# Kernel optimization log

Measured on AMD Instinct MI355X. Metric: run time of the kernel, lower is better.

The kernel has to match this reference:

```python
import jax, jax.numpy as jnp
import numpy as np

N = 8192   # nodes per modality
D = 128    # hidden_channels
H = 2      # transformer heads
R = 15     # relations in HeteroConv (use_speaker='no')
E = 16384  # edges per relation
L = 2      # num_layers
# relation src/dst node-type ids: 0=audio, 1=text, 2=visual (dict order: a/v/t past, a/v/t future, a/v/t self, then cross)
SRC = np.array([0, 2, 1, 0, 2, 1, 0, 2, 1, 0, 0, 2, 2, 1, 1])
DST = np.array([0, 2, 1, 0, 2, 1, 0, 2, 1, 2, 1, 0, 1, 0, 2])


def setup_inputs() -> dict:
    key = jax.random.key(0)
    ks = jax.random.split(key, 18)
    f = lambda k, sh: jax.random.normal(k, sh, dtype=jnp.float32) * 0.05
    return {
        "x_audio": jax.random.normal(ks[0], (N, D), jnp.float32),
        "x_text": jax.random.normal(ks[1], (N, D), jnp.float32),
        "x_visual": jax.random.normal(ks[2], (N, D), jnp.float32),
        "edge_index": jax.random.randint(ks[3], (R, 2, E), 0, N, jnp.int32),
        "Wrel": f(ks[4], (L, R, D, D)),
        "brel": f(ks[5], (L, R, D)),
        "Wroot": f(ks[6], (L, R, D, D)),
        "Wq": f(ks[7], (D, H * D)), "bq": f(ks[8], (H * D,)),
        "Wk": f(ks[9], (D, H * D)), "bk": f(ks[10], (H * D,)),
        "Wv": f(ks[11], (D, H * D)), "bv": f(ks[12], (H * D,)),
        "Wskip": f(ks[13], (D, D)), "bskip": f(ks[14], (D,)),
        "gamma": jnp.ones((D,), jnp.float32),
        "beta": jnp.zeros((D,), jnp.float32),
    }


def reference(x_audio, x_text, x_visual, edge_index, Wrel, brel, Wroot,
              Wq, bq, Wk, bk, Wv, bv, Wskip, bskip, gamma, beta):
    src_t = jnp.asarray(SRC)
    dst_t = jnp.asarray(DST)
    x = jnp.stack([x_audio, x_text, x_visual])           # [3, N, D]
    src_idx = edge_index[:, 0]                            # [R, E]
    dst_idx = edge_index[:, 1]                            # [R, E]
    rel = jnp.arange(R)

    # --- HeteroConv of 15 GraphConvs (aggr='add' inside, 'mean' over the 5 relations per dst type) ---
    seg = (rel[:, None] * N + dst_idx).reshape(-1)        # per-relation segment ids
    for l in range(L):
        feats = jnp.take_along_axis(x[src_t], src_idx[:, :, None], axis=1)     # [R, E, D]
        msg = jax.ops.segment_sum(feats.reshape(R * E, D), seg,
                                  num_segments=R * N).reshape(R, N, D)          # scatter-add per relation
        out = (jnp.einsum('rnd,rde->rne', msg, Wrel[l]) + brel[l][:, None, :]
               + jnp.einsum('rnd,rde->rne', x[dst_t], Wroot[l]))                # lin_rel(agg) + lin_root(x_dst)
        x = jax.nn.relu(jnp.zeros_like(x).at[dst_t].add(out) / 5.0)            # mean over 5 relations per dst

    # --- hetero_to_homo: concat audio, text, visual (offsets 0, N, 2N) ---
    hx = x.reshape(3 * N, D)
    src_h = (src_t[:, None] * N + src_idx).reshape(-1)    # [R*E]
    dst_h = (dst_t[:, None] * N + dst_idx).reshape(-1)

    # --- TransformerConv (concat=False -> head mean, root skip) ---
    q = (hx @ Wq + bq).reshape(3 * N, H, D)
    k = (hx @ Wk + bk).reshape(3 * N, H, D)
    v = (hx @ Wv + bv).reshape(3 * N, H, D)
    logits = jnp.einsum('ehd,ehd->eh', q[dst_h], k[src_h]) / jnp.sqrt(jnp.float32(D))
    m = jax.ops.segment_max(logits, dst_h, num_segments=3 * N)
    p = jnp.exp(logits - m[dst_h])
    denom = jax.ops.segment_sum(p, dst_h, num_segments=3 * N)
    alpha = p / denom[dst_h]                              # segment softmax over incoming edges
    agg = jax.ops.segment_sum(alpha[:, :, None] * v[src_h], dst_h, num_segments=3 * N)  # [3N, H, D]
    out = agg.mean(axis=1) + hx @ Wskip + bskip

    # --- BatchNorm1d (training-mode batch stats) + leaky_relu ---
    mu = out.mean(axis=0)
    var = ((out - mu) ** 2).mean(axis=0)
    y = (out - mu) / jnp.sqrt(var + 1e-5) * gamma + beta
    y = jax.nn.leaky_relu(y)                              # negative_slope=0.01 (torch default)
    return y.reshape(3, N, D)                             # [audio, text, visual]
```

## Files before the change

kernel.cpp:

```cpp
#include <hip/hip_runtime.h>
#include <hip/hip_bf16.h>

#define NN 8192
#define DD 128
#define HH 2
#define RR 15
#define EE 16384
#define NLAYER 2
#define NMOD 3
#define TN (NMOD*NN)
#define NE (RR*EE)
#define SCB (TN/256)

#define SRC_BITS 0x16818618u
#define DST_BITS 0x21198618u
__device__ __forceinline__ int srcOf(int r) { return (SRC_BITS >> (2 * r)) & 3; }
__device__ __forceinline__ int dstOf(int r) { return (DST_BITS >> (2 * r)) & 3; }

typedef __attribute__((ext_vector_type(8))) short bf16x8;
typedef __attribute__((ext_vector_type(4))) float f32x4;
typedef _Float16 h2 __attribute__((ext_vector_type(2)));

__device__ __forceinline__ unsigned short f2bf(float v) {
    union { float f; unsigned int u; } x; x.f = v;
    unsigned int r = (x.u + 0x7fffu + ((x.u >> 16) & 1u)) >> 16;
    return (unsigned short)r;
}
__device__ __forceinline__ float bf2f(unsigned int bits16) {
    return __uint_as_float(bits16 << 16);
}
__device__ __forceinline__ void bfu4(uint4 u, float* f) {
    f[0] = bf2f(u.x & 0xffffu); f[1] = bf2f(u.x >> 16);
    f[2] = bf2f(u.y & 0xffffu); f[3] = bf2f(u.y >> 16);
    f[4] = bf2f(u.z & 0xffffu); f[5] = bf2f(u.z >> 16);
    f[6] = bf2f(u.w & 0xffffu); f[7] = bf2f(u.w >> 16);
}

__device__ __forceinline__ float dot8_f16(uint4 a, uint4 b, float acc) {
#if __has_builtin(__builtin_amdgcn_fdot2)
    acc = __builtin_amdgcn_fdot2(__builtin_bit_cast(h2, a.x), __builtin_bit_cast(h2, b.x), acc, false);
    acc = __builtin_amdgcn_fdot2(__builtin_bit_cast(h2, a.y), __builtin_bit_cast(h2, b.y), acc, false);
    acc = __builtin_amdgcn_fdot2(__builtin_bit_cast(h2, a.z), __builtin_bit_cast(h2, b.z), acc, false);
    acc = __builtin_amdgcn_fdot2(__builtin_bit_cast(h2, a.w), __builtin_bit_cast(h2, b.w), acc, false);
#else
    h2 av, bv;
    av = __builtin_bit_cast(h2, a.x); bv = __builtin_bit_cast(h2, b.x);
    acc += (float)av.x * (float)bv.x + (float)av.y * (float)bv.y;
    av = __builtin_bit_cast(h2, a.y); bv = __builtin_bit_cast(h2, b.y);
    acc += (float)av.x * (float)bv.x + (float)av.y * (float)bv.y;
    av = __builtin_bit_cast(h2, a.z); bv = __builtin_bit_cast(h2, b.z);
    acc += (float)av.x * (float)bv.x + (float)av.y * (float)bv.y;
    av = __builtin_bit_cast(h2, a.w); bv = __builtin_bit_cast(h2, b.w);
    acc += (float)av.x * (float)bv.x + (float)av.y * (float)bv.y;
#endif
    return acc;
}

__global__ __launch_bounds__(256) void prep_all(
        const float* __restrict__ Wrel, const float* __restrict__ Wroot,
        const float* __restrict__ brel,
        const float* __restrict__ Wq, const float* __restrict__ Wk,
        const float* __restrict__ Wv, const float* __restrict__ Wskip,
        const float* __restrict__ xa, const float* __restrict__ xt,
        const float* __restrict__ xv,
        unsigned short* __restrict__ WrelT, unsigned short* __restrict__ WsumT,
        float* __restrict__ bsum,
        unsigned short* __restrict__ WqT, unsigned short* __restrict__ WkT,
        unsigned short* __restrict__ WvT, unsigned short* __restrict__ WskipT,
        unsigned short* __restrict__ xb, int* __restrict__ cnt) {
    int y = blockIdx.y;
    int t = blockIdx.x * 256 + threadIdx.x;
    if (y < 30) {
        int k = t >> 7, c = t & 127;
        WrelT[(size_t)y * 16384 + c * 128 + k] = f2bf(Wrel[(size_t)y * 16384 + t]);
    } else if (y < 36) {
        int mat = y - 30, l = mat / 3, m = mat % 3;
        int k = t >> 7, c = t & 127;
        float s = 0.f;
        #pragma unroll
        for (int r = 0; r < RR; r++)
            if (((DST_BITS >> (2 * r)) & 3) == (unsigned)m) s += Wroot[(size_t)(l * RR + r) * 16384 + t];
        WsumT[(size_t)mat * 16384 + c * 128 + k] = f2bf(s);
        if (blockIdx.x == 0 && threadIdx.x < 128) {
            float b = 0.f;
            #pragma unroll
            for (int r = 0; r < RR; r++)
                if (((DST_BITS >> (2 * r)) & 3) == (unsigned)m) b += brel[(l * RR + r) * 128 + threadIdx.x];
            bsum[mat * 128 + threadIdx.x] = b;
        }
    } else if (y < 39) {
        int which = y - 36;
        const float* s = which == 0 ? Wq : which == 1 ? Wk : Wv;
        unsigned short* d = which == 0 ? WqT : which == 1 ? WkT : WvT;
        #pragma unroll
        for (int it = 0; it < 2; it++) {
            int tt = t + it * 16384;
            int k = tt >> 8, c = tt & 255;
            d[c * 128 + k] = f2bf(s[tt]);
        }
    } else if (y == 39) {
        int k = t >> 7, c = t & 127;
        WskipT[c * 128 + k] = f2bf(Wskip[t]);
    } else if (y == 40) {
        for (int i = t; i < TN + 256; i += 16384) cnt[i] = 0;
    } else {
        int m = y - 41;
        const float* s = m == 0 ? xa : m == 1 ? xt : xv;
        unsigned short* d = xb + (size_t)m * NN * DD;
        for (int i = t * 4; i < NN * DD; i += 16384 * 4) {
            float4 v = *(const float4*)(s + i);
            uint2 o;
            o.x = (unsigned)f2bf(v.x) | ((unsigned)f2bf(v.y) << 16);
            o.y = (unsigned)f2bf(v.z) | ((unsigned)f2bf(v.w) << 16);
            *(uint2*)(d + i) = o;
        }
    }
}

__global__ void count_edges(const int* __restrict__ edge, int* __restrict__ cnt) {
    int t = blockIdx.x * 256 + threadIdx.x;
    if (t >= NE) return;
    int r = t >> 14, e = t & (EE - 1);
    int dst = edge[r * 2 * EE + EE + e];
    atomicAdd(&cnt[dstOf(r) * NN + dst], 1);
}

__global__ __launch_bounds__(256) void scan_reduce(const int* __restrict__ cnt,
                                                   int* __restrict__ part) {
    int t = threadIdx.x;
    int v = cnt[blockIdx.x * 256 + t];
    #pragma unroll
    for (int off = 32; off >= 1; off >>= 1) v += __shfl_xor(v, off);
    __shared__ int ws[4];
    if ((t & 63) == 0) ws[t >> 6] = v;
    __syncthreads();
    if (t == 0) part[blockIdx.x] = ws[0] + ws[1] + ws[2] + ws[3];
}

__global__ __launch_bounds__(128) void scan_mid(int* __restrict__ part, int* __restrict__ startA) {
    __shared__ int lds[128];
    int t = threadIdx.x;
    int v = (t < SCB) ? part[t] : 0;
    lds[t] = v;
    __syncthreads();
    for (int off = 1; off < 128; off <<= 1) {
        int u = (t >= off) ? lds[t - off] : 0;
        __syncthreads();
        lds[t] += u;
        __syncthreads();
    }
    if (t < SCB) part[t] = lds[t] - v;
    if (t == 0) startA[TN] = NE;
}

__global__ __launch_bounds__(256) void scan_final(const int* __restrict__ cnt,
                                                  const int* __restrict__ part,
                                                  int* __restrict__ startA,
                                                  int* __restrict__ cursor) {
    int t = threadIdx.x;
    int lane = t & 63, w = t >> 6;
    int i = blockIdx.x * 256 + t;
    int v = cnt[i];
    int inc = v;
    #pragma unroll
    for (int off = 1; off < 64; off <<= 1) {
        int u = __shfl_up(inc, off);
        if (lane >= off) inc += u;
    }
    __shared__ int wtot[4];
    if (lane == 63) wtot[w] = inc;
    __syncthreads();
    int wofs = 0;
    #pragma unroll
    for (int j = 0; j < 4; j++) if (j < w) wofs += wtot[j];
    int ex = part[blockIdx.x] + wofs + inc - v;
    startA[i] = ex;
    cursor[i] = ex;
}

__global__ void place_edges(const int* __restrict__ edge, int* __restrict__ cursor,
                            unsigned int* __restrict__ sorted) {
    int t = blockIdx.x * 256 + threadIdx.x;
    if (t >= NE) return;
    int r = t >> 14, e = t & (EE - 1);
    int src = edge[r * 2 * EE + e];
    int dst = edge[r * 2 * EE + EE + e];
    int pos = atomicAdd(&cursor[dstOf(r) * NN + dst], 1);
    unsigned int zrow = ((unsigned int)r << 13) | (unsigned int)src;
    unsigned int srch = (unsigned int)(srcOf(r) * NN + src);
    sorted[pos] = (zrow << 15) | srch;
}

template<int MODE>
__device__ __forceinline__ void gemm_tile(const unsigned short* __restrict__ A,
                                          const unsigned short* __restrict__ BT,
                                          const float* __restrict__ bias,
                                          void* __restrict__ Cout,
                                          int ldc, int colofs, int row0,
                                          unsigned short* lds, float oscale = 1.f) {
    unsigned short* Alds = lds;
    unsigned short* Blds = lds + 16384;
    const int tid = threadIdx.x;
    const int lane = tid & 63;
    const int w = tid >> 6;
    #pragma unroll
    for (int i = 0; i < 8; i++) {
        int c = i * 256 + tid;
        int row = c >> 4;
        int k0 = (c & 15) << 3;
        uint4 va = *(const uint4*)(A + (size_t)(row0 + row) * 128 + k0);
        *(uint4*)((char*)Alds + (((row * 256 + k0 * 2)) ^ ((row & 7) << 4))) = va;
        uint4 vb = *(const uint4*)(BT + (size_t)row * 128 + k0);
        *(uint4*)((char*)Blds + (((row * 256 + k0 * 2)) ^ ((row & 7) << 4))) = vb;
    }
    __syncthreads();
    f32x4 acc[2][8];
    #pragma unroll
    for (int mi = 0; mi < 2; mi++)
        #pragma unroll
        for (int nj = 0; nj < 8; nj++) acc[mi][nj] = (f32x4){0.f, 0.f, 0.f, 0.f};
    const int lr = lane & 15, lk = lane >> 4;
    #pragma unroll
    for (int ks = 0; ks < 4; ks++) {
        bf16x8 a[2], b[8];
        #pragma unroll
        for (int mi = 0; mi < 2; mi++) {
            int row = w * 32 + mi * 16 + lr;
            a[mi] = *(const bf16x8*)((char*)Alds + ((row * 256 + (ks * 32 + lk * 8) * 2) ^ ((row & 7) << 4)));
        }
        #pragma unroll
        for (int nj = 0; nj < 8; nj++) {
            int row = nj * 16 + lr;
            b[nj] = *(const bf16x8*)((char*)Blds + ((row * 256 + (ks * 32 + lk * 8) * 2) ^ ((row & 7) << 4)));
        }
        #pragma unroll
        for (int mi = 0; mi < 2; mi++)
            #pragma unroll
            for (int nj = 0; nj < 8; nj++)
                acc[mi][nj] = __builtin_amdgcn_mfma_f32_16x16x32_bf16(a[mi], b[nj], acc[mi][nj], 0, 0, 0);
    }
    __syncthreads();
    float* Clds = (float*)lds;
    #pragma unroll
    for (int mi = 0; mi < 2; mi++) {
        #pragma unroll
        for (int nj = 0; nj < 8; nj++) {
            int ccl = nj * 16 + lr;
            float bb = bias ? bias[ccl] : 0.f;
            #pragma unroll
            for (int r = 0; r < 4; r++) {
                int row = w * 32 + mi * 16 + lk * 4 + r;
                Clds[row * 128 + ccl] = acc[mi][nj][r] + bb;
            }
        }
    }
    __syncthreads();
    #pragma unroll
    for (int p = 0; p < 8; p++) {
        int row = p * 16 + (tid >> 4);
        int c0 = (tid & 15) * 8;
        float4 fa = *(const float4*)(Clds + row * 128 + c0);
        float4 fb = *(const float4*)(Clds + row * 128 + c0 + 4);
        if (MODE == 2) {
            unsigned r0 = (unsigned)f2bf(fa.x) | ((unsigned)f2bf(fa.y) << 16);
            unsigned r1 = (unsigned)f2bf(fa.z) | ((unsigned)f2bf(fa.w) << 16);
            unsigned r2 = (unsigned)f2bf(fb.x) | ((unsigned)f2bf(fb.y) << 16);
            unsigned r3 = (unsigned)f2bf(fb.z) | ((unsigned)f2bf(fb.w) << 16);
            uint4 pk = {r0, r1, r2, r3};
            *(uint4*)((unsigned short*)Cout + (size_t)(row0 + row) * ldc + colofs + c0) = pk;
        } else if (MODE == 3) {
            unsigned r0 = __builtin_bit_cast(unsigned, __builtin_amdgcn_cvt_pkrtz(fa.x * oscale, fa.y * oscale));
            unsigned r1 = __builtin_bit_cast(unsigned, __builtin_amdgcn_cvt_pkrtz(fa.z * oscale, fa.w * oscale));
            unsigned r2 = __builtin_bit_cast(unsigned, __builtin_amdgcn_cvt_pkrtz(fb.x * oscale, fb.y * oscale));
            unsigned r3 = __builtin_bit_cast(unsigned, __builtin_amdgcn_cvt_pkrtz(fb.z * oscale, fb.w * oscale));
            uint4 pk = {r0, r1, r2, r3};
            *(uint4*)((unsigned short*)Cout + (size_t)(row0 + row) * ldc + colofs + c0) = pk;
        } else {
            float* Cf = (float*)Cout;
            *(float4*)(Cf + (size_t)(row0 + row) * ldc + colofs + c0) = fa;
            *(float4*)(Cf + (size_t)(row0 + row) * ldc + colofs + c0 + 4) = fb;
        }
    }
}

__global__ __launch_bounds__(256) void zroot_gemm(const unsigned short* __restrict__ xbf,
                                                  const unsigned short* __restrict__ WrelT_l,
                                                  const unsigned short* __restrict__ WrootSumT_l,
                                                  const float* __restrict__ brelSum_l,
                                                  unsigned short* __restrict__ z,
                                                  unsigned short* __restrict__ xroot) {
    __shared__ unsigned short lds[2 * 16384];
    int y = blockIdx.y;
    if (y < RR) {
        gemm_tile<2>(xbf + (size_t)srcOf(y) * NN * 128, WrelT_l + (size_t)y * 16384, nullptr,
                     z + (size_t)y * NN * 128, 128, 0, blockIdx.x * 128, lds);
    } else {
        int m = y - RR;
        gemm_tile<2>(xbf + (size_t)m * NN * 128, WrootSumT_l + (size_t)m * 16384, brelSum_l + m * 128,
                     xroot + (size_t)m * NN * 128, 128, 0, blockIdx.x * 128, lds);
    }
}

__global__ __launch_bounds__(256) void qkvskip_gemm(const unsigned short* __restrict__ xbf,
                                                    const unsigned short* __restrict__ WqT,
                                                    const unsigned short* __restrict__ WkT,
                                                    const unsigned short* __restrict__ WvT,
                                                    const unsigned short* __restrict__ WskipT,
                                                    const float* __restrict__ bq,
                                                    const float* __restrict__ bk,
                                                    const float* __restrict__ bv,
                                                    const float* __restrict__ bskip,
                                                    unsigned short* __restrict__ qb,
                                                    unsigned short* __restrict__ kb,
                                                    unsigned short* __restrict__ vb,
                                                    float* __restrict__ out) {
    __shared__ unsigned short lds[2 * 16384];
    int y = blockIdx.y;
    if (y < 4) {
        int which = y >> 1, half = y & 1;
        const unsigned short* BT = (which == 0 ? WqT : WkT) + half * 16384;
        const float* bias = (which == 0 ? bq : bk) + half * 128;
        unsigned short* C = (which == 0 ? qb : kb);
        float os = (which == 0) ? 0.08838834764831845f : 1.f;
        gemm_tile<3>(xbf, BT, bias, C, 256, half * 128, blockIdx.x * 128, lds, os);
    } else if (y < 6) {
        int half = y & 1;
        gemm_tile<2>(xbf, WvT + half * 16384, bv + half * 128, vb, 256, half * 128, blockIdx.x * 128, lds);
    } else {
        gemm_tile<0>(xbf, WskipT, bskip, out, 128, 0, blockIdx.x * 128, lds);
    }
}

__global__ __launch_bounds__(256) void gather_relu(const unsigned short* __restrict__ z,
                                                   const unsigned short* __restrict__ xroot,
                                                   const unsigned int* __restrict__ sorted,
                                                   const int* __restrict__ startA,
                                                   unsigned short* __restrict__ xout) {
    int node = blockIdx.x * 4 + (threadIdx.x >> 6);
    int lane = threadIdx.x & 63;
    int g = lane >> 4, p = lane & 15;
    int st = startA[node], en = startA[node + 1];
    float acc[8];
    #pragma unroll
    for (int j = 0; j < 8; j++) acc[j] = 0.f;
    int idx = st + g;
    unsigned int vcur = (idx < en) ? sorted[idx] : 0u;
    for (int base = st; base < en; base += 4) {
        unsigned int vnext = (idx + 4 < en) ? sorted[idx + 4] : 0u;
        uint4 u = *(const uint4*)(z + ((size_t)(vcur >> 15) << 7) + p * 8);
        if (idx < en) {
            float f[8]; bfu4(u, f);
            #pragma unroll
            for (int j = 0; j < 8; j++) acc[j] += f[j];
        }
        vcur = vnext;
        idx += 4;
    }
    #pragma unroll
    for (int j = 0; j < 8; j++) {
        acc[j] += __shfl_xor(acc[j], 32);
        acc[j] += __shfl_xor(acc[j], 16);
    }
    if (g == 0) {
        uint4 rt = *(const uint4*)(xroot + ((size_t)node << 7) + p * 8);
        float r[8]; bfu4(rt, r);
        unsigned short o[8];
        #pragma unroll
        for (int j = 0; j < 8; j++) {
            float v = (r[j] + acc[j]) * 0.2f;
            o[j] = f2bf(v > 0.f ? v : 0.f);
        }
        uint4 pk;
        pk.x = (unsigned)o[0] | ((unsigned)o[1] << 16);
        pk.y = (unsigned)o[2] | ((unsigned)o[3] << 16);
        pk.z = (unsigned)o[4] | ((unsigned)o[5] << 16);
        pk.w = (unsigned)o[6] | ((unsigned)o[7] << 16);
        *(uint4*)(xout + ((size_t)node << 7) + p * 8) = pk;
    }
}

__global__ __launch_bounds__(256) void attn_fused(const unsigned short* __restrict__ qb,
                                                  const unsigned short* __restrict__ kb,
                                                  const unsigned short* __restrict__ vb,
                                                  const unsigned int* __restrict__ sorted,
                                                  const int* __restrict__ startA,
                                                  float* __restrict__ out) {
    int node = blockIdx.x * 4 + (threadIdx.x >> 6);
    int lane = threadIdx.x & 63;
    int g = lane >> 4, p = lane & 15;
    uint4 q0 = *(const uint4*)(qb + (size_t)node * 256 + p * 8);
    uint4 q1 = *(const uint4*)(qb + (size_t)node * 256 + 128 + p * 8);
    float s0 = 0.f, s1 = 0.f;
    float a0[8], a1[8];
    #pragma unroll
    for (int j = 0; j < 8; j++) { a0[j] = 0.f; a1[j] = 0.f; }
    int st = startA[node], en = startA[node + 1];
    int idx = st + g;
    unsigned int vcur = (idx < en) ? sorted[idx] : 0u;
    for (int base = st; base < en; base += 4) {
        unsigned int vnext = (idx + 4 < en) ? sorted[idx + 4] : 0u;
        bool valid = idx < en;
        int srch = (int)(vcur & 32767u);
        const unsigned short* krow = kb + (size_t)srch * 256;
        const unsigned short* vrow = vb + (size_t)srch * 256;
        uint4 k0r = *(const uint4*)(krow + p * 8);
        uint4 k1r = *(const uint4*)(krow + 128 + p * 8);
        uint4 v0r = *(const uint4*)(vrow + p * 8);
        uint4 v1r = *(const uint4*)(vrow + 128 + p * 8);
        float d0 = dot8_f16(q0, k0r, 0.f);
        float d1 = dot8_f16(q1, k1r, 0.f);
        #pragma unroll
        for (int off = 8; off >= 1; off >>= 1) {
            d0 += __shfl_xor(d0, off);
            d1 += __shfl_xor(d1, off);
        }
        float p0 = valid ? __expf(d0) : 0.f;
        float p1 = valid ? __expf(d1) : 0.f;
        s0 += p0; s1 += p1;
        float v0[8], v1[8];
        bfu4(v0r, v0); bfu4(v1r, v1);
        #pragma unroll
        for (int j = 0; j < 8; j++) {
            a0[j] += p0 * v0[j];
            a1[j] += p1 * v1[j];
        }
        vcur = vnext;
        idx += 4;
    }
    #pragma unroll
    for (int off = 32; off >= 16; off >>= 1) {
        s0 += __shfl_xor(s0, off);
        s1 += __shfl_xor(s1, off);
        #pragma unroll
        for (int j = 0; j < 8; j++) {
            a0[j] += __shfl_xor(a0[j], off);
            a1[j] += __shfl_xor(a1[j], off);
        }
    }
    if (g == 0) {
        float inv0 = (s0 > 0.f) ? 0.5f / s0 : 0.f;
        float inv1 = (s1 > 0.f) ? 0.5f / s1 : 0.f;
        float* op = out + (size_t)node * 128 + p * 8;
        float4 ska = *(const float4*)op;
        float4 skb = *(const float4*)(op + 4);
        float4 ra, rb;
        ra.x = a0[0] * inv0 + a1[0] * inv1 + ska.x;
        ra.y = a0[1] * inv0 + a1[1] * inv1 + ska.y;
        ra.z = a0[2] * inv0 + a1[2] * inv1 + ska.z;
        ra.w = a0[3] * inv0 + a1[3] * inv1 + ska.w;
        rb.x = a0[4] * inv0 + a1[4] * inv1 + skb.x;
        rb.y = a0[5] * inv0 + a1[5] * inv1 + skb.y;
        rb.z = a0[6] * inv0 + a1[6] * inv1 + skb.z;
        rb.w = a0[7] * inv0 + a1[7] * inv1 + skb.w;
        *(float4*)op = ra;
        *(float4*)(op + 4) = rb;
    }
}

__global__ void colstats(const float* __restrict__ outb, float* __restrict__ stats) {
    int col = threadIdx.x & 127;
    int sub = threadIdx.x >> 7;
    float s = 0.f, ss = 0.f;
    for (int row = blockIdx.x * 2 + sub; row < TN; row += gridDim.x * 2) {
        float vv = outb[(size_t)row * DD + col];
        s += vv;
        ss += vv * vv;
    }
    __shared__ float red[2][256];
    red[0][threadIdx.x] = s;
    red[1][threadIdx.x] = ss;
    __syncthreads();
    if (sub == 0) {
        s  += red[0][threadIdx.x + 128];
        ss += red[1][threadIdx.x + 128];
        atomicAdd(&stats[col], s);
        atomicAdd(&stats[DD + col], ss);
    }
}

__global__ void ln_act(float* __restrict__ outb, const float* __restrict__ stats,
                       const float* __restrict__ gamma, const float* __restrict__ beta) {
    int i = (blockIdx.x * 256 + threadIdx.x) * 4;
    if (i >= TN * DD) return;
    int col = i & 127;
    float4 v = *(const float4*)(outb + i);
    float o[4] = {v.x, v.y, v.z, v.w};
    #pragma unroll
    for (int j = 0; j < 4; j++) {
        int c = col + j;
        float mu = stats[c] * (1.f / TN);
        float var = stats[DD + c] * (1.f / TN) - mu * mu;
        float inv = rsqrtf(var + 1e-5f);
        float vv = (o[j] - mu) * inv * gamma[c] + beta[c];
        o[j] = vv > 0.f ? vv : 0.01f * vv;
    }
    float4 res = {o[0], o[1], o[2], o[3]};
    *(float4*)(outb + i) = res;
}

extern "C" void kernel_launch(void* const* d_in, const int* in_sizes, int n_in,
                              void* d_out, int out_size, void* d_ws, size_t ws_size,
                              hipStream_t stream) {
    const float* x_audio = (const float*)d_in[0];
    const float* x_text  = (const float*)d_in[1];
    const float* x_vis   = (const float*)d_in[2];
    const int*   edge    = (const int*)d_in[3];
    const float* Wrel    = (const float*)d_in[4];
    const float* brel    = (const float*)d_in[5];
    const float* Wroot   = (const float*)d_in[6];
    const float* Wq      = (const float*)d_in[7];
    const float* bq      = (const float*)d_in[8];
    const float* Wk      = (const float*)d_in[9];
    const float* bk      = (const float*)d_in[10];
    const float* Wv      = (const float*)d_in[11];
    const float* bv      = (const float*)d_in[12];
    const float* Wskip   = (const float*)d_in[13];
    const float* bskip   = (const float*)d_in[14];
    const float* gamma   = (const float*)d_in[15];
    const float* beta    = (const float*)d_in[16];
    float* out = (float*)d_out;

    char* p = (char*)d_ws;
    unsigned short* xbfA = (unsigned short*)p; p += (size_t)TN * 128 * 2;
    unsigned short* xbfB = (unsigned short*)p; p += (size_t)TN * 128 * 2;
    unsigned short* zqkv = (unsigned short*)p; p += (size_t)3 * TN * 256 * 2;
    unsigned short* z  = zqkv;
    unsigned short* qb = zqkv;
    unsigned short* kb = zqkv + (size_t)TN * 256;
    unsigned short* vb = zqkv + (size_t)2 * TN * 256;
    unsigned short* xroot = (unsigned short*)p; p += (size_t)TN * 128 * 2;
    unsigned short* WrelT = (unsigned short*)p; p += (size_t)2 * RR * 16384 * 2;
    unsigned short* WrootSumT = (unsigned short*)p; p += (size_t)6 * 16384 * 2;
    float* brelSum = (float*)p; p += 6 * 128 * 4;
    unsigned short* WqT = (unsigned short*)p; p += 256 * 128 * 2;
    unsigned short* WkT = (unsigned short*)p; p += 256 * 128 * 2;
    unsigned short* WvT = (unsigned short*)p; p += 256 * 128 * 2;
    unsigned short* WskipT = (unsigned short*)p; p += 128 * 128 * 2;
    unsigned int* sorted = (unsigned int*)p; p += (size_t)NE * 4;
    int* startA = (int*)p; p += (TN + 4) * 4;
    int* cursor = (int*)p; p += (TN + 4) * 4;
    int* cnt = (int*)p; p += TN * 4;
    float* stats = (float*)p; p += 256 * 4;
    int* part = (int*)p; p += SCB * 4;
    size_t needed = (size_t)(p - (char*)d_ws);
    if (ws_size < needed) return;

    prep_all<<<dim3(64, 44), 256, 0, stream>>>(Wrel, Wroot, brel, Wq, Wk, Wv, Wskip,
                                               x_audio, x_text, x_vis,
                                               WrelT, WrootSumT, brelSum,
                                               WqT, WkT, WvT, WskipT, xbfA, cnt);

    count_edges<<<NE / 256, 256, 0, stream>>>(edge, cnt);
    scan_reduce<<<SCB, 256, 0, stream>>>(cnt, part);
    scan_mid<<<1, 128, 0, stream>>>(part, startA);
    scan_final<<<SCB, 256, 0, stream>>>(cnt, part, startA, cursor);
    place_edges<<<NE / 256, 256, 0, stream>>>(edge, cursor, sorted);

    unsigned short* xcur = xbfA;
    unsigned short* xnxt = xbfB;
    for (int l = 0; l < NLAYER; ++l) {
        zroot_gemm<<<dim3(NN / 128, RR + NMOD), 256, 0, stream>>>(
            xcur, WrelT + (size_t)l * RR * 16384, WrootSumT + (size_t)l * NMOD * 16384,
            brelSum + l * NMOD * 128, z, xroot);
        gather_relu<<<TN / 4, 256, 0, stream>>>(z, xroot, sorted, startA, xnxt);
        unsigned short* t = xcur; xcur = xnxt; xnxt = t;
    }

    qkvskip_gemm<<<dim3(TN / 128, 7), 256, 0, stream>>>(xcur, WqT, WkT, WvT, WskipT,
                                                        bq, bk, bv, bskip, qb, kb, vb, out);
    attn_fused<<<TN / 4, 256, 0, stream>>>(qb, kb, vb, sorted, startA, out);

    colstats<<<384, 256, 0, stream>>>(out, stats);
    ln_act<<<(TN * DD) / 1024, 256, 0, stream>>>(out, stats, gamma, beta);
}
```

Before: 202.2 us.

## Switch bf16 storage to fp16, fold edge counting and scan-mid into neighbors

```diff
diff --git a/kernel.cpp b/kernel.cpp
--- a/kernel.cpp
+++ b/kernel.cpp
@@ -17,23 +17,15 @@
 __device__ __forceinline__ int srcOf(int r) { return (SRC_BITS >> (2 * r)) & 3; }
 __device__ __forceinline__ int dstOf(int r) { return (DST_BITS >> (2 * r)) & 3; }
 
-typedef __attribute__((ext_vector_type(8))) short bf16x8;
+typedef __attribute__((ext_vector_type(8))) _Float16 f16x8;
 typedef __attribute__((ext_vector_type(4))) float f32x4;
 typedef _Float16 h2 __attribute__((ext_vector_type(2)));
 
-__device__ __forceinline__ unsigned short f2bf(float v) {
-    union { float f; unsigned int u; } x; x.f = v;
-    unsigned int r = (x.u + 0x7fffu + ((x.u >> 16) & 1u)) >> 16;
-    return (unsigned short)r;
-}
-__device__ __forceinline__ float bf2f(unsigned int bits16) {
-    return __uint_as_float(bits16 << 16);
-}
-__device__ __forceinline__ void bfu4(uint4 u, float* f) {
-    f[0] = bf2f(u.x & 0xffffu); f[1] = bf2f(u.x >> 16);
-    f[2] = bf2f(u.y & 0xffffu); f[3] = bf2f(u.y >> 16);
-    f[4] = bf2f(u.z & 0xffffu); f[5] = bf2f(u.z >> 16);
-    f[6] = bf2f(u.w & 0xffffu); f[7] = bf2f(u.w >> 16);
+__device__ __forceinline__ unsigned short f2h(float v) {
+    return __builtin_bit_cast(unsigned short, (_Float16)v);
+}
+__device__ __forceinline__ unsigned int pkh(float a, float b) {
+    return __builtin_bit_cast(unsigned int, __builtin_amdgcn_cvt_pkrtz(a, b));
 }
 
 __device__ __forceinline__ float dot8_f16(uint4 a, uint4 b, float acc) {
@@ -56,13 +48,17 @@
     return acc;
 }
 
+__device__ __forceinline__ h2 h2shfl_xor(h2 a, int off) {
+    return __builtin_bit_cast(h2, __shfl_xor(__builtin_bit_cast(int, a), off));
+}
+
 __global__ __launch_bounds__(256) void prep_all(
         const float* __restrict__ Wrel, const float* __restrict__ Wroot,
         const float* __restrict__ brel,
         const float* __restrict__ Wq, const float* __restrict__ Wk,
         const float* __restrict__ Wv, const float* __restrict__ Wskip,
         const float* __restrict__ xa, const float* __restrict__ xt,
-        const float* __restrict__ xv,
+        const float* __restrict__ xv, const int* __restrict__ edge,
         unsigned short* __restrict__ WrelT, unsigned short* __restrict__ WsumT,
         float* __restrict__ bsum,
         unsigned short* __restrict__ WqT, unsigned short* __restrict__ WkT,
@@ -72,7 +68,7 @@
     int t = blockIdx.x * 256 + threadIdx.x;
     if (y < 30) {
         int k = t >> 7, c = t & 127;
-        WrelT[(size_t)y * 16384 + c * 128 + k] = f2bf(Wrel[(size_t)y * 16384 + t]);
+        WrelT[(size_t)y * 16384 + c * 128 + k] = f2h(Wrel[(size_t)y * 16384 + t]);
     } else if (y < 36) {
         int mat = y - 30, l = mat / 3, m = mat % 3;
         int k = t >> 7, c = t & 127;
@@ -80,7 +76,7 @@
         #pragma unroll
         for (int r = 0; r < RR; r++)
             if (((DST_BITS >> (2 * r)) & 3) == (unsigned)m) s += Wroot[(size_t)(l * RR + r) * 16384 + t];
-        WsumT[(size_t)mat * 16384 + c * 128 + k] = f2bf(s);
+        WsumT[(size_t)mat * 16384 + c * 128 + k] = f2h(s);
         if (blockIdx.x == 0 && threadIdx.x < 128) {
             float b = 0.f;
             #pragma unroll
@@ -96,33 +92,28 @@
         for (int it = 0; it < 2; it++) {
             int tt = t + it * 16384;
             int k = tt >> 8, c = tt & 255;
-            d[c * 128 + k] = f2bf(s[tt]);
+            d[c * 128 + k] = f2h(s[tt]);
         }
     } else if (y == 39) {
         int k = t >> 7, c = t & 127;
-        WskipT[c * 128 + k] = f2bf(Wskip[t]);
-    } else if (y == 40) {
-        for (int i = t; i < TN + 256; i += 16384) cnt[i] = 0;
-    } else {
-        int m = y - 41;
+        WskipT[c * 128 + k] = f2h(Wskip[t]);
+    } else if (y < 43) {
+        int m = y - 40;
         const float* s = m == 0 ? xa : m == 1 ? xt : xv;
         unsigned short* d = xb + (size_t)m * NN * DD;
         for (int i = t * 4; i < NN * DD; i += 16384 * 4) {
             float4 v = *(const float4*)(s + i);
             uint2 o;
-            o.x = (unsigned)f2bf(v.x) | ((unsigned)f2bf(v.y) << 16);
-            o.y = (unsigned)f2bf(v.z) | ((unsigned)f2bf(v.w) << 16);
+            o.x = pkh(v.x, v.y);
+            o.y = pkh(v.z, v.w);
             *(uint2*)(d + i) = o;
         }
-    }
-}
-
-__global__ void count_edges(const int* __restrict__ edge, int* __restrict__ cnt) {
-    int t = blockIdx.x * 256 + threadIdx.x;
-    if (t >= NE) return;
-    int r = t >> 14, e = t & (EE - 1);
-    int dst = edge[r * 2 * EE + EE + e];
-    atomicAdd(&cnt[dstOf(r) * NN + dst], 1);
+    } else {
+        int id = (y - 43) * 16384 + t;
+        int r = id >> 14, e = id & (EE - 1);
+        int dst = edge[r * 2 * EE + EE + e];
+        atomicAdd(&cnt[dstOf(r) * NN + dst], 1);
+    }
 }
 
 __global__ __launch_bounds__(256) void scan_reduce(const int* __restrict__ cnt,
@@ -137,28 +128,20 @@
     if (t == 0) part[blockIdx.x] = ws[0] + ws[1] + ws[2] + ws[3];
 }
 
-__global__ __launch_bounds__(128) void scan_mid(int* __restrict__ part, int* __restrict__ startA) {
-    __shared__ int lds[128];
-    int t = threadIdx.x;
-    int v = (t < SCB) ? part[t] : 0;
-    lds[t] = v;
-    __syncthreads();
-    for (int off = 1; off < 128; off <<= 1) {
-        int u = (t >= off) ? lds[t - off] : 0;
-        __syncthreads();
-        lds[t] += u;
-        __syncthreads();
-    }
-    if (t < SCB) part[t] = lds[t] - v;
-    if (t == 0) startA[TN] = NE;
-}
-
 __global__ __launch_bounds__(256) void scan_final(const int* __restrict__ cnt,
                                                   const int* __restrict__ part,
                                                   int* __restrict__ startA,
                                                   int* __restrict__ cursor) {
+    __shared__ int pofs;
     int t = threadIdx.x;
     int lane = t & 63, w = t >> 6;
+    if (t < 64) {
+        int s = 0;
+        for (int j = t; j < SCB; j += 64) s += (j < (int)blockIdx.x) ? part[j] : 0;
+        #pragma unroll
+        for (int off = 32; off >= 1; off >>= 1) s += __shfl_xor(s, off);
+        if (t == 0) pofs = s;
+    }
     int i = blockIdx.x * 256 + t;
     int v = cnt[i];
     int inc = v;
@@ -173,9 +156,10 @@
     int wofs = 0;
     #pragma unroll
     for (int j = 0; j < 4; j++) if (j < w) wofs += wtot[j];
-    int ex = part[blockIdx.x] + wofs + inc - v;
+    int ex = pofs + wofs + inc - v;
     startA[i] = ex;
     cursor[i] = ex;
+    if (i == TN - 1) startA[TN] = NE;
 }
 
 __global__ void place_edges(const int* __restrict__ edge, int* __restrict__ cursor,
@@ -222,22 +206,22 @@
     const int lr = lane & 15, lk = lane >> 4;
     #pragma unroll
     for (int ks = 0; ks < 4; ks++) {
-        bf16x8 a[2], b[8];
+        f16x8 a[2], b[8];
         #pragma unroll
         for (int mi = 0; mi < 2; mi++) {
             int row = w * 32 + mi * 16 + lr;
-            a[mi] = *(const bf16x8*)((char*)Alds + ((row * 256 + (ks * 32 + lk * 8) * 2) ^ ((row & 7) << 4)));
+            a[mi] = *(const f16x8*)((char*)Alds + ((row * 256 + (ks * 32 + lk * 8) * 2) ^ ((row & 7) << 4)));
         }
         #pragma unroll
         for (int nj = 0; nj < 8; nj++) {
             int row = nj * 16 + lr;
-            b[nj] = *(const bf16x8*)((char*)Blds + ((row * 256 + (ks * 32 + lk * 8) * 2) ^ ((row & 7) << 4)));
+            b[nj] = *(const f16x8*)((char*)Blds + ((row * 256 + (ks * 32 + lk * 8) * 2) ^ ((row & 7) << 4)));
         }
         #pragma unroll
         for (int mi = 0; mi < 2; mi++)
             #pragma unroll
             for (int nj = 0; nj < 8; nj++)
-                acc[mi][nj] = __builtin_amdgcn_mfma_f32_16x16x32_bf16(a[mi], b[nj], acc[mi][nj], 0, 0, 0);
+                acc[mi][nj] = __builtin_amdgcn_mfma_f32_16x16x32_f16(a[mi], b[nj], acc[mi][nj], 0, 0, 0);
     }
     __syncthreads();
     float* Clds = (float*)lds;
@@ -261,19 +245,12 @@
         int c0 = (tid & 15) * 8;
         float4 fa = *(const float4*)(Clds + row * 128 + c0);
         float4 fb = *(const float4*)(Clds + row * 128 + c0 + 4);
-        if (MODE == 2) {
-            unsigned r0 = (unsigned)f2bf(fa.x) | ((unsigned)f2bf(fa.y) << 16);
-            unsigned r1 = (unsigned)f2bf(fa.z) | ((unsigned)f2bf(fa.w) << 16);
-            unsigned r2 = (unsigned)f2bf(fb.x) | ((unsigned)f2bf(fb.y) << 16);
-            unsigned r3 = (unsigned)f2bf(fb.z) | ((unsigned)f2bf(fb.w) << 16);
-            uint4 pk = {r0, r1, r2, r3};
-            *(uint4*)((unsigned short*)Cout + (size_t)(row0 + row) * ldc + colofs + c0) = pk;
-        } else if (MODE == 3) {
-            unsigned r0 = __builtin_bit_cast(unsigned, __builtin_amdgcn_cvt_pkrtz(fa.x * oscale, fa.y * oscale));
-            unsigned r1 = __builtin_bit_cast(unsigned, __builtin_amdgcn_cvt_pkrtz(fa.z * oscale, fa.w * oscale));
-            unsigned r2 = __builtin_bit_cast(unsigned, __builtin_amdgcn_cvt_pkrtz(fb.x * oscale, fb.y * oscale));
-            unsigned r3 = __builtin_bit_cast(unsigned, __builtin_amdgcn_cvt_pkrtz(fb.z * oscale, fb.w * oscale));
-            uint4 pk = {r0, r1, r2, r3};
+        if (MODE == 3) {
+            uint4 pk;
+            pk.x = pkh(fa.x * oscale, fa.y * oscale);
+            pk.y = pkh(fa.z * oscale, fa.w * oscale);
+            pk.z = pkh(fb.x * oscale, fb.y * oscale);
+            pk.w = pkh(fb.z * oscale, fb.w * oscale);
             *(uint4*)((unsigned short*)Cout + (size_t)(row0 + row) * ldc + colofs + c0) = pk;
         } else {
             float* Cf = (float*)Cout;
@@ -292,11 +269,11 @@
     __shared__ unsigned short lds[2 * 16384];
     int y = blockIdx.y;
     if (y < RR) {
-        gemm_tile<2>(xbf + (size_t)srcOf(y) * NN * 128, WrelT_l + (size_t)y * 16384, nullptr,
+        gemm_tile<3>(xbf + (size_t)srcOf(y) * NN * 128, WrelT_l + (size_t)y * 16384, nullptr,
                      z + (size_t)y * NN * 128, 128, 0, blockIdx.x * 128, lds);
     } else {
         int m = y - RR;
-        gemm_tile<2>(xbf + (size_t)m * NN * 128, WrootSumT_l + (size_t)m * 16384, brelSum_l + m * 128,
+        gemm_tile<3>(xbf + (size_t)m * NN * 128, WrootSumT_l + (size_t)m * 16384, brelSum_l + m * 128,
                      xroot + (size_t)m * NN * 128, 128, 0, blockIdx.x * 128, lds);
     }
 }
@@ -316,16 +293,13 @@
                                                     float* __restrict__ out) {
     __shared__ unsigned short lds[2 * 16384];
     int y = blockIdx.y;
-    if (y < 4) {
+    if (y < 6) {
         int which = y >> 1, half = y & 1;
-        const unsigned short* BT = (which == 0 ? WqT : WkT) + half * 16384;
-        const float* bias = (which == 0 ? bq : bk) + half * 128;
-        unsigned short* C = (which == 0 ? qb : kb);
+        const unsigned short* BT = (which == 0 ? WqT : which == 1 ? WkT : WvT) + half * 16384;
+        const float* bias = (which == 0 ? bq : which == 1 ? bk : bv) + half * 128;
+        unsigned short* C = (which == 0 ? qb : which == 1 ? kb : vb);
         float os = (which == 0) ? 0.08838834764831845f : 1.f;
         gemm_tile<3>(xbf, BT, bias, C, 256, half * 128, blockIdx.x * 128, lds, os);
-    } else if (y < 6) {
-        int half = y & 1;
-        gemm_tile<2>(xbf, WvT + half * 16384, bv + half * 128, vb, 256, half * 128, blockIdx.x * 128, lds);
     } else {
         gemm_tile<0>(xbf, WskipT, bskip, out, 128, 0, blockIdx.x * 128, lds);
     }
@@ -340,41 +314,43 @@
     int lane = threadIdx.x & 63;
     int g = lane >> 4, p = lane & 15;
     int st = startA[node], en = startA[node + 1];
-    float acc[8];
-    #pragma unroll
-    for (int j = 0; j < 8; j++) acc[j] = 0.f;
+    h2 acc[4];
+    #pragma unroll
+    for (int j = 0; j < 4; j++) acc[j] = (h2){0, 0};
     int idx = st + g;
     unsigned int vcur = (idx < en) ? sorted[idx] : 0u;
     for (int base = st; base < en; base += 4) {
         unsigned int vnext = (idx + 4 < en) ? sorted[idx + 4] : 0u;
         uint4 u = *(const uint4*)(z + ((size_t)(vcur >> 15) << 7) + p * 8);
         if (idx < en) {
-            float f[8]; bfu4(u, f);
-            #pragma unroll
-            for (int j = 0; j < 8; j++) acc[j] += f[j];
+            acc[0] += __builtin_bit_cast(h2, u.x);
+            acc[1] += __builtin_bit_cast(h2, u.y);
+            acc[2] += __builtin_bit_cast(h2, u.z);
+            acc[3] += __builtin_bit_cast(h2, u.w);
         }
         vcur = vnext;
         idx += 4;
     }
     #pragma unroll
-    for (int j = 0; j < 8; j++) {
-        acc[j] += __shfl_xor(acc[j], 32);
-        acc[j] += __shfl_xor(acc[j], 16);
+    for (int j = 0; j < 4; j++) {
+        acc[j] += h2shfl_xor(acc[j], 32);
+        acc[j] += h2shfl_xor(acc[j], 16);
     }
     if (g == 0) {
         uint4 rt = *(const uint4*)(xroot + ((size_t)node << 7) + p * 8);
-        float r[8]; bfu4(rt, r);
-        unsigned short o[8];
-        #pragma unroll
-        for (int j = 0; j < 8; j++) {
-            float v = (r[j] + acc[j]) * 0.2f;
-            o[j] = f2bf(v > 0.f ? v : 0.f);
-        }
+        h2 r[4];
+        r[0] = __builtin_bit_cast(h2, rt.x);
+        r[1] = __builtin_bit_cast(h2, rt.y);
+        r[2] = __builtin_bit_cast(h2, rt.z);
+        r[3] = __builtin_bit_cast(h2, rt.w);
         uint4 pk;
-        pk.x = (unsigned)o[0] | ((unsigned)o[1] << 16);
-        pk.y = (unsigned)o[2] | ((unsigned)o[3] << 16);
-        pk.z = (unsigned)o[4] | ((unsigned)o[5] << 16);
-        pk.w = (unsigned)o[6] | ((unsigned)o[7] << 16);
+        unsigned int* po = (unsigned int*)&pk;
+        #pragma unroll
+        for (int j = 0; j < 4; j++) {
+            float v0 = ((float)r[j].x + (float)acc[j].x) * 0.2f;
+            float v1 = ((float)r[j].y + (float)acc[j].y) * 0.2f;
+            po[j] = pkh(v0 > 0.f ? v0 : 0.f, v1 > 0.f ? v1 : 0.f);
+        }
         *(uint4*)(xout + ((size_t)node << 7) + p * 8) = pk;
     }
 }
@@ -391,9 +367,9 @@
     uint4 q0 = *(const uint4*)(qb + (size_t)node * 256 + p * 8);
     uint4 q1 = *(const uint4*)(qb + (size_t)node * 256 + 128 + p * 8);
     float s0 = 0.f, s1 = 0.f;
-    float a0[8], a1[8];
-    #pragma unroll
-    for (int j = 0; j < 8; j++) { a0[j] = 0.f; a1[j] = 0.f; }
+    h2 a0h[4], a1h[4];
+    #pragma unroll
+    for (int jj = 0; jj < 4; jj++) { a0h[jj] = (h2){0, 0}; a1h[jj] = (h2){0, 0}; }
     int st = startA[node], en = startA[node + 1];
     int idx = st + g;
     unsigned int vcur = (idx < en) ? sorted[idx] : 0u;
@@ -417,13 +393,16 @@
         float p0 = valid ? __expf(d0) : 0.f;
         float p1 = valid ? __expf(d1) : 0.f;
         s0 += p0; s1 += p1;
-        float v0[8], v1[8];
-        bfu4(v0r, v0); bfu4(v1r, v1);
-        #pragma unroll
-        for (int j = 0; j < 8; j++) {
-            a0[j] += p0 * v0[j];
-            a1[j] += p1 * v1[j];
-        }
+        h2 ph0 = (h2){(_Float16)p0, (_Float16)p0};
+        h2 ph1 = (h2){(_Float16)p1, (_Float16)p1};
+        a0h[0] += ph0 * __builtin_bit_cast(h2, v0r.x);
+        a0h[1] += ph0 * __builtin_bit_cast(h2, v0r.y);
+        a0h[2] += ph0 * __builtin_bit_cast(h2, v0r.z);
+        a0h[3] += ph0 * __builtin_bit_cast(h2, v0r.w);
+        a1h[0] += ph1 * __builtin_bit_cast(h2, v1r.x);
+        a1h[1] += ph1 * __builtin_bit_cast(h2, v1r.y);
+        a1h[2] += ph1 * __builtin_bit_cast(h2, v1r.z);
+        a1h[3] += ph1 * __builtin_bit_cast(h2, v1r.w);
         vcur = vnext;
         idx += 4;
     }
@@ -432,14 +411,20 @@
         s0 += __shfl_xor(s0, off);
         s1 += __shfl_xor(s1, off);
         #pragma unroll
-        for (int j = 0; j < 8; j++) {
-            a0[j] += __shfl_xor(a0[j], off);
-            a1[j] += __shfl_xor(a1[j], off);
+        for (int jj = 0; jj < 4; jj++) {
+            a0h[jj] += h2shfl_xor(a0h[jj], off);
+            a1h[jj] += h2shfl_xor(a1h[jj], off);
         }
     }
     if (g == 0) {
         float inv0 = (s0 > 0.f) ? 0.5f / s0 : 0.f;
         float inv1 = (s1 > 0.f) ? 0.5f / s1 : 0.f;
+        float a0[8], a1[8];
+        #pragma unroll
+        for (int jj = 0; jj < 4; jj++) {
+            a0[2 * jj] = (float)a0h[jj].x; a0[2 * jj + 1] = (float)a0h[jj].y;
+            a1[2 * jj] = (float)a1h[jj].x; a1[2 * jj + 1] = (float)a1h[jj].y;
+        }
         float* op = out + (size_t)node * 128 + p * 8;
         float4 ska = *(const float4*)op;
         float4 skb = *(const float4*)(op + 4);
@@ -545,14 +530,13 @@
     size_t needed = (size_t)(p - (char*)d_ws);
     if (ws_size < needed) return;
 
-    prep_all<<<dim3(64, 44), 256, 0, stream>>>(Wrel, Wroot, brel, Wq, Wk, Wv, Wskip,
-                                               x_audio, x_text, x_vis,
+    hipMemsetAsync(cnt, 0, (TN + 256) * 4, stream);
+    prep_all<<<dim3(64, 58), 256, 0, stream>>>(Wrel, Wroot, brel, Wq, Wk, Wv, Wskip,
+                                               x_audio, x_text, x_vis, edge,
                                                WrelT, WrootSumT, brelSum,
                                                WqT, WkT, WvT, WskipT, xbfA, cnt);
 
-    count_edges<<<NE / 256, 256, 0, stream>>>(edge, cnt);
     scan_reduce<<<SCB, 256, 0, stream>>>(cnt, part);
-    scan_mid<<<1, 128, 0, stream>>>(part, startA);
     scan_final<<<SCB, 256, 0, stream>>>(cnt, part, startA, cursor);
     place_edges<<<NE / 256, 256, 0, stream>>>(edge, cursor, sorted);
 
```

After: 201.3 us. No clear change (-0.4%).
